# Kernel optimization log

Hardware: AMD Instinct MI355X
Metric: run time of the kernel (lower is better)

Reference implementation:

```python
import jax, jax.numpy as jnp
import numpy as np

STATE_DIM = 256
ACT_LEN = 128
INPUT_DIM = STATE_DIM + 2 * ACT_LEN
B_SZ, T = 32, 2048
SLOPE = 0.01


def leaky(x):
    return jnp.where(x < 0, SLOPE * x, x)


def inv_leaky(x):
    return jnp.where(x < 0, x / SLOPE, x)


def _lin_init(key, out_d, in_d):
    k1, k2 = jax.random.split(key)
    bound = 1.0 / np.sqrt(in_d)
    W = jax.random.uniform(k1, (out_d, in_d), minval=-bound, maxval=bound, dtype=jnp.float32)
    b = jax.random.uniform(k2, (out_d,), minval=-bound, maxval=bound, dtype=jnp.float32)
    return W, b


def setup_inputs() -> dict:
    key = jax.random.key(0)
    ks = jax.random.split(key, 8)
    padded_input = jax.random.normal(ks[0], (B_SZ, T, INPUT_DIM), dtype=jnp.float32)
    We1, be1 = _lin_init(ks[1], STATE_DIM, STATE_DIM)
    We2, be2 = _lin_init(ks[2], STATE_DIM, STATE_DIM)
    A_W, A_b = _lin_init(ks[3], STATE_DIM, STATE_DIM)
    B_W, B_b = _lin_init(ks[4], STATE_DIM, ACT_LEN)
    Wd1, bd1 = _lin_init(ks[5], STATE_DIM, STATE_DIM)
    Wd2, bd2 = _lin_init(ks[6], STATE_DIM, STATE_DIM)
    return {"padded_input": padded_input, "We1": We1, "be1": be1, "We2": We2, "be2": be2,
            "A_W": A_W, "A_b": A_b, "B_W": B_W, "B_b": B_b,
            "Wd1": Wd1, "bd1": bd1, "Wd2": Wd2, "bd2": bd2}


def reference(padded_input, We1, be1, We2, be2, A_W, A_b, B_W, B_b, Wd1, bd1, Wd2, bd2):
    x_t = padded_input[:, :, :STATE_DIM]                      # [B,T,D]
    u_t = padded_input[:, :, STATE_DIM:STATE_DIM + ACT_LEN]   # [B,T,A]
    # encoder: (Linear + LeakyReLU) x 2
    z = leaky(jnp.einsum('btd,ed->bte', x_t, We1) + be1)
    z = leaky(jnp.einsum('btd,ed->bte', z, We2) + be2)
    # recurrence z_{t} uses encoded state only at t=0 (reset_probability=0, nwarmup=0)
    Bu = jnp.einsum('bta,da->btd', u_t, B_W) + B_b            # [B,T,D], precomputed
    z0 = z[:, 0, :]                                           # [B,D]

    def step(carry, bu_t):
        out = jnp.einsum('bd,ed->be', carry, A_W) + A_b + bu_t
        return out, out

    _, z1 = jax.lax.scan(step, z0, jnp.swapaxes(Bu, 0, 1))    # z1: [T,B,D]
    z1 = jnp.swapaxes(z1, 0, 1)                               # [B,T,D]
    # decoder: (InverseLeakyReLU + Linear) x 2
    y = jnp.einsum('btd,ed->bte', inv_leaky(z1), Wd1) + bd1
    y = jnp.einsum('btd,ed->bte', inv_leaky(y), Wd2) + bd2
    return y
```

## Files before the change

kernel.cpp:

```cpp
#include <hip/hip_runtime.h>

#define D256 256
#define ALEN 128
#define INDIM 512
#define BSZ 32
#define TLEN 2048
#define CHL 32
#define NCH 64

typedef __attribute__((ext_vector_type(8))) short short8;
typedef __attribute__((ext_vector_type(4))) float f32x4;

__device__ __forceinline__ float leakyf(float x)  { return x < 0.f ? 0.01f * x : x; }
__device__ __forceinline__ float ileakyf(float x) { return x < 0.f ? x * 100.0f : x; }

__device__ __forceinline__ unsigned short f2bf(float f) {
  unsigned int x = __float_as_uint(f);
  unsigned int r = x + 0x7FFFu + ((x >> 16) & 1u);
  return (unsigned short)(r >> 16);
}

__device__ __forceinline__ float bf2f(unsigned short u) {
  return __uint_as_float(((unsigned int)u) << 16);
}

__device__ __forceinline__ void gload16(const void* g, const void* l) {
  __builtin_amdgcn_global_load_lds(
      (const __attribute__((address_space(1))) unsigned int*)g,
      (__attribute__((address_space(3))) unsigned int*)l, 16, 0, 0);
}

template <int CTRL>
__device__ __forceinline__ float dpp_addf(float x) {
  return x + __int_as_float(__builtin_amdgcn_update_dpp(
                 0, __float_as_int(x), CTRL, 0xF, 0xF, true));
}
__device__ __forceinline__ void red8(float4& s) {
  s.x = dpp_addf<0xB1>(s.x); s.y = dpp_addf<0xB1>(s.y);
  s.z = dpp_addf<0xB1>(s.z); s.w = dpp_addf<0xB1>(s.w);
  s.x = dpp_addf<0x4E>(s.x); s.y = dpp_addf<0x4E>(s.y);
  s.z = dpp_addf<0x4E>(s.z); s.w = dpp_addf<0x4E>(s.w);
  s.x = dpp_addf<0x141>(s.x); s.y = dpp_addf<0x141>(s.y);
  s.z = dpp_addf<0x141>(s.z); s.w = dpp_addf<0x141>(s.w);
}

__global__ __launch_bounds__(256) void gemm_mfma(
    const unsigned short* __restrict__ In, int K,
    const unsigned short* __restrict__ W,
    const float* __restrict__ bias1, const float* __restrict__ bias2,
    int ileaky_act, int out_bf16, void* __restrict__ Outp) {
  __shared__ char lds[16384];
  const int tid = threadIdx.x;
  const int lane = tid & 63, w = tid >> 6;
  const int m0 = blockIdx.x * 128, n0 = blockIdx.y * 128;
  const int wm = (w & 1) * 64, wn = (w >> 1) * 64;
  const int quad = lane >> 4, l16 = lane & 15;

  f32x4 acc[4][4];
#pragma unroll
  for (int i = 0; i < 4; ++i)
#pragma unroll
    for (int j = 0; j < 4; ++j) acc[i][j] = {0.f, 0.f, 0.f, 0.f};

  for (int kb = 0; kb < K; kb += 32) {
    __syncthreads();
#pragma unroll
    for (int q = 0; q < 2; ++q) {
      const int id = (w * 2 + q) * 64 + lane;
      const int row = id >> 2, ch = id & 3;
      gload16(In + (size_t)(m0 + row) * K + kb + ch * 8,
              lds + (w * 2 + q) * 1024);
      gload16(W + (size_t)(n0 + row) * K + kb + ch * 8,
              lds + 8192 + (w * 2 + q) * 1024);
    }
    __syncthreads();

    short8 af[4], bf[4];
#pragma unroll
    for (int i = 0; i < 4; ++i) {
      af[i] = *(const short8*)(lds + ((wm + i * 16 + l16) * 64 + quad * 16));
      bf[i] = *(const short8*)(lds + 8192 + ((wn + i * 16 + l16) * 64 + quad * 16));
    }
#pragma unroll
    for (int i = 0; i < 4; ++i)
#pragma unroll
      for (int j = 0; j < 4; ++j)
        acc[i][j] = __builtin_amdgcn_mfma_f32_16x16x32_bf16(af[i], bf[j], acc[i][j], 0, 0, 0);
  }

#pragma unroll
  for (int j = 0; j < 4; ++j) {
    const int n = n0 + wn + j * 16 + l16;
    const float bv = (bias1 ? bias1[n] : 0.f) + (bias2 ? bias2[n] : 0.f);
#pragma unroll
    for (int i = 0; i < 4; ++i) {
#pragma unroll
      for (int r = 0; r < 4; ++r) {
        const int m = m0 + wm + i * 16 + quad * 4 + r;
        float v = acc[i][j][r] + bv;
        if (ileaky_act) v = ileakyf(v);
        if (out_bf16)
          ((unsigned short*)Outp)[(size_t)m * 256 + n] = f2bf(v);
        else
          ((float*)Outp)[(size_t)m * 256 + n] = v;
      }
    }
  }
}

__global__ __launch_bounds__(256) void gemm_corr(
    const unsigned short* __restrict__ Eb, const unsigned short* __restrict__ Mb,
    const float* __restrict__ Df, unsigned short* __restrict__ w1) {
  __shared__ char lds[16384];
  const int tid = threadIdx.x;
  const int lane = tid & 63, w = tid >> 6;
  const int m0 = blockIdx.x * 128, n0 = blockIdx.y * 128;
  const int wm = (w & 1) * 64, wn = (w >> 1) * 64;
  const int quad = lane >> 4, l16 = lane & 15;

  f32x4 acc[4][4];
#pragma unroll
  for (int i = 0; i < 4; ++i)
#pragma unroll
    for (int j = 0; j < 4; ++j) acc[i][j] = {0.f, 0.f, 0.f, 0.f};

  for (int kb = 0; kb < 256; kb += 32) {
    __syncthreads();
#pragma unroll
    for (int q = 0; q < 2; ++q) {
      const int id = (w * 2 + q) * 64 + lane;
      const int row = id >> 2, ch = id & 3;
      gload16(Eb + (size_t)(m0 + row) * 256 + kb + ch * 8,
              lds + (w * 2 + q) * 1024);
      gload16(Mb + (size_t)(n0 + row) * 256 + kb + ch * 8,
              lds + 8192 + (w * 2 + q) * 1024);
    }
    __syncthreads();

    short8 af[4], bf[4];
#pragma unroll
    for (int i = 0; i < 4; ++i) {
      af[i] = *(const short8*)(lds + ((wm + i * 16 + l16) * 64 + quad * 16));
      bf[i] = *(const short8*)(lds + 8192 + ((wn + i * 16 + l16) * 64 + quad * 16));
    }
#pragma unroll
    for (int i = 0; i < 4; ++i)
#pragma unroll
      for (int j = 0; j < 4; ++j)
        acc[i][j] = __builtin_amdgcn_mfma_f32_16x16x32_bf16(af[i], bf[j], acc[i][j], 0, 0, 0);
  }

#pragma unroll
  for (int jf = 0; jf < 4; ++jf) {
    const int n = n0 + wn + jf * 16 + l16;
    const int jj = n >> 8, e = n & 255;
#pragma unroll
    for (int i = 0; i < 4; ++i) {
#pragma unroll
      for (int r = 0; r < 4; ++r) {
        const int m = m0 + wm + i * 16 + quad * 4 + r;
        const int kk = m >> 5, bb = m & 31;
        const size_t addr = ((size_t)bb * TLEN + (size_t)kk * CHL + jj) * 256 + e;
        float v = acc[i][jf][r] + Df[addr];
        w1[addr] = f2bf(ileakyf(v));
      }
    }
  }
}

__global__ __launch_bounds__(256) void gemm_pow(
    const float* __restrict__ P, const float* __restrict__ XTb,
    float* __restrict__ OutS, float* __restrict__ OutST,
    unsigned short* __restrict__ OutSb) {
  __shared__ float a_lds[64][40];
  __shared__ float b_lds[64][40];
  const size_t zo = (size_t)blockIdx.z << 16;
  const float* XT = XTb + zo;
  const int tid = threadIdx.x;
  const int tm = tid >> 4, tn = tid & 15;
  const int m0 = blockIdx.x * 64, n0 = blockIdx.y * 64;
  float acc[4][4];
#pragma unroll
  for (int i = 0; i < 4; ++i)
#pragma unroll
    for (int j = 0; j < 4; ++j) acc[i][j] = 0.f;

  for (int kb = 0; kb < 256; kb += 32) {
    __syncthreads();
#pragma unroll
    for (int q = 0; q < 2; ++q) {
      const int slot = q * 256 + tid;
      const int row = slot >> 3, s4 = slot & 7;
      *(float4*)&a_lds[row][s4 * 4] = *(const float4*)&P[(size_t)(m0 + row) * 256 + kb + s4 * 4];
      *(float4*)&b_lds[row][s4 * 4] = *(const float4*)&XT[(size_t)(n0 + row) * 256 + kb + s4 * 4];
    }
    __syncthreads();
#pragma unroll
    for (int k4 = 0; k4 < 8; ++k4) {
      float4 a4[4], b4[4];
#pragma unroll
      for (int i = 0; i < 4; ++i) a4[i] = *(const float4*)&a_lds[tm * 4 + i][k4 * 4];
#pragma unroll
      for (int j = 0; j < 4; ++j) b4[j] = *(const float4*)&b_lds[tn * 4 + j][k4 * 4];
#pragma unroll
      for (int i = 0; i < 4; ++i)
#pragma unroll
        for (int j = 0; j < 4; ++j)
          acc[i][j] += a4[i].x * b4[j].x + a4[i].y * b4[j].y +
                       a4[i].z * b4[j].z + a4[i].w * b4[j].w;
    }
  }
  float* Out = OutS + zo;
  float* OutT = OutST + zo;
  unsigned short* Ob = OutSb + zo;
#pragma unroll
  for (int i = 0; i < 4; ++i) {
    const int m = m0 + tm * 4 + i;
    float4 v = make_float4(acc[i][0], acc[i][1], acc[i][2], acc[i][3]);
    *(float4*)&Out[(size_t)m * 256 + n0 + tn * 4] = v;
    *(ushort4*)&Ob[(size_t)m * 256 + n0 + tn * 4] =
        make_ushort4(f2bf(v.x), f2bf(v.y), f2bf(v.z), f2bf(v.w));
#pragma unroll
    for (int j = 0; j < 4; ++j)
      OutT[(size_t)(n0 + tn * 4 + j) * 256 + m] = acc[i][j];
  }
}

__global__ __launch_bounds__(256) void prep_kernel(
    const float* __restrict__ in, const float* __restrict__ We1,
    const float* __restrict__ be1, const float* __restrict__ We2,
    const float* __restrict__ be2, const float* __restrict__ A_W,
    const float* __restrict__ B_W, const float* __restrict__ Wd1,
    const float* __restrict__ Wd2, float* __restrict__ AT0,
    unsigned short* __restrict__ Ab0, float* __restrict__ z0,
    unsigned short* __restrict__ BWb, unsigned short* __restrict__ Wd1b,
    unsigned short* __restrict__ Wd2b) {
  __shared__ float sm[1056];
  const int tid = threadIdx.x;
  const int blk = blockIdx.x;
  if (blk < 64) {
    const int bx = (blk & 7) * 32, by = (blk >> 3) * 32;
    const int lx = tid & 31, ly = tid >> 5;
#pragma unroll
    for (int i = 0; i < 4; ++i) {
      const float v = A_W[(size_t)(by + ly + 8 * i) * 256 + bx + lx];
      sm[(ly + 8 * i) * 33 + lx] = v;
      Ab0[(size_t)(by + ly + 8 * i) * 256 + bx + lx] = f2bf(v);
    }
    __syncthreads();
#pragma unroll
    for (int i = 0; i < 4; ++i)
      AT0[(size_t)(bx + ly + 8 * i) * 256 + by + lx] = sm[lx * 33 + ly + 8 * i];
  } else if (blk < 96) {
    const int b = blk - 64, e = tid;
    float* xb = sm;
    float* h1 = sm + 256;
    xb[e] = in[(size_t)b * TLEN * INDIM + e];
    __syncthreads();
    float acc = be1[e];
    const float4* w = (const float4*)(We1 + (size_t)e * 256);
#pragma unroll 8
    for (int d4 = 0; d4 < 64; ++d4) {
      float4 wv = w[d4];
      acc += wv.x * xb[4 * d4] + wv.y * xb[4 * d4 + 1] + wv.z * xb[4 * d4 + 2] + wv.w * xb[4 * d4 + 3];
    }
    h1[e] = leakyf(acc);
    __syncthreads();
    float a2 = be2[e];
    w = (const float4*)(We2 + (size_t)e * 256);
#pragma unroll 8
    for (int d4 = 0; d4 < 64; ++d4) {
      float4 wv = w[d4];
      a2 += wv.x * h1[4 * d4] + wv.y * h1[4 * d4 + 1] + wv.z * h1[4 * d4 + 2] + wv.w * h1[4 * d4 + 3];
    }
    z0[(size_t)b * 256 + e] = leakyf(a2);
  } else {
    const float* src;
    unsigned short* dst;
    int i4;
    if (blk < 128)      { src = B_W; dst = BWb;  i4 = (blk - 96) * 256 + tid; }
    else if (blk < 192) { src = Wd1; dst = Wd1b; i4 = (blk - 128) * 256 + tid; }
    else                { src = Wd2; dst = Wd2b; i4 = (blk - 192) * 256 + tid; }
    float4 v = *(const float4*)&src[(size_t)i4 * 4];
    *(ushort4*)&dst[(size_t)i4 * 4] =
        make_ushort4(f2bf(v.x), f2bf(v.y), f2bf(v.z), f2bf(v.w));
  }
}

__global__ __launch_bounds__(256) void extract_u(const float* __restrict__ in,
                                                 unsigned short* __restrict__ ubuf) {
  const int gid = blockIdx.x * 256 + threadIdx.x;
  const int row = gid >> 5;
  const int c = (gid & 31) * 4;
  float4 v = *(const float4*)&in[(size_t)row * INDIM + 256 + c];
  *(ushort4*)&ubuf[(size_t)row * 128 + c] =
      make_ushort4(f2bf(v.x), f2bf(v.y), f2bf(v.z), f2bf(v.w));
}

__global__ __launch_bounds__(512, 2) void phase_kernel(
    const float* __restrict__ AW, float* __restrict__ Cbuf,
    float* __restrict__ Lend) {
  const int tid = threadIdx.x;
  const int w = tid >> 6;
  const int lane = tid & 63;
  const int dg = lane & 7;
  const int le = lane >> 3;
  const int e0 = w * 32 + le * 4;
  const int d0 = dg * 32;
  const int rho0 = blockIdx.x << 3;
  const int k = rho0 >> 5;
  const int b = (rho0 & 31) + dg;
  const int rho = rho0 + dg;

  __shared__ __align__(16) float carry[2][8][292];

  float4 Ar[4][8];
#pragma unroll
  for (int i = 0; i < 4; ++i)
#pragma unroll
    for (int k4 = 0; k4 < 8; ++k4)
      Ar[i][k4] = *(const float4*)&AW[(size_t)(e0 + i) * 256 + d0 + k4 * 4];

  float4 cur = make_float4(0.f, 0.f, 0.f, 0.f);
  const int epad = e0 + ((e0 >> 5) << 2);
  *(float4*)&carry[0][dg][epad] = cur;
  __syncthreads();

  float4* crow = (float4*)(Cbuf + ((size_t)b * TLEN + (size_t)k * CHL) * 256 + e0);

  int buf = 0;
  for (int j = 0; j < CHL; ++j) {
    const float4 cj = *crow;
    float4 s[8];
#pragma unroll
    for (int r = 0; r < 8; ++r) s[r] = make_float4(0.f, 0.f, 0.f, 0.f);
#pragma unroll
    for (int k4 = 0; k4 < 8; ++k4) {
      const float4 a0 = Ar[0][k4], a1 = Ar[1][k4], a2 = Ar[2][k4], a3 = Ar[3][k4];
#pragma unroll
      for (int r = 0; r < 8; ++r) {
        const float4 cv = *(const float4*)&carry[buf][r][dg * 36 + k4 * 4];
        s[r].x += a0.x * cv.x + a0.y * cv.y + a0.z * cv.z + a0.w * cv.w;
        s[r].y += a1.x * cv.x + a1.y * cv.y + a1.z * cv.z + a1.w * cv.w;
        s[r].z += a2.x * cv.x + a2.y * cv.y + a2.z * cv.z + a2.w * cv.w;
        s[r].w += a3.x * cv.x + a3.y * cv.y + a3.z * cv.z + a3.w * cv.w;
      }
    }
    float4 nxt = make_float4(0.f, 0.f, 0.f, 0.f);
#pragma unroll
    for (int r = 0; r < 8; ++r) {
      red8(s[r]);
      if (dg == r) nxt = s[r];
    }
    cur = make_float4(nxt.x + cj.x, nxt.y + cj.y, nxt.z + cj.z, nxt.w + cj.w);
    buf ^= 1;
    *(float4*)&carry[buf][dg][epad] = cur;
    *crow = cur;
    crow += 64;
    __syncthreads();
  }
  *(float4*)&Lend[(size_t)rho * 256 + e0] = cur;
}

__global__ __launch_bounds__(512, 2) void boundary_kernel(
    const float* __restrict__ P, const float* __restrict__ z0,
    const float* __restrict__ Lend, unsigned short* __restrict__ Eb) {
  const int tid = threadIdx.x;
  const int w = tid >> 6;
  const int lane = tid & 63;
  const int dg = lane & 7;
  const int le = lane >> 3;
  const int e0 = w * 32 + le * 4;
  const int d0 = dg * 32;
  const int b = blockIdx.x;

  __shared__ __align__(16) float Ec[292];

  float4 Pr[4][8];
#pragma unroll
  for (int i = 0; i < 4; ++i)
#pragma unroll
    for (int k4 = 0; k4 < 8; ++k4)
      Pr[i][k4] = *(const float4*)&P[(size_t)(e0 + i) * 256 + d0 + k4 * 4];

  float4 cur = *(const float4*)&z0[(size_t)b * 256 + e0];
  const int epad = e0 + ((e0 >> 5) << 2);
  if (dg == 0) *(float4*)&Ec[epad] = cur;
  __syncthreads();

  for (int k = 0; k < NCH; ++k) {
    const float4 lv = *(const float4*)&Lend[((size_t)k * BSZ + b) * 256 + e0];
    if (dg == 0)
      *(ushort4*)&Eb[((size_t)k * BSZ + b) * 256 + e0] =
          make_ushort4(f2bf(cur.x), f2bf(cur.y), f2bf(cur.z), f2bf(cur.w));

    float4 s = make_float4(0.f, 0.f, 0.f, 0.f);
#pragma unroll
    for (int k4 = 0; k4 < 8; ++k4) {
      const float4 cv = *(const float4*)&Ec[dg * 36 + k4 * 4];
      s.x += Pr[0][k4].x * cv.x + Pr[0][k4].y * cv.y + Pr[0][k4].z * cv.z + Pr[0][k4].w * cv.w;
      s.y += Pr[1][k4].x * cv.x + Pr[1][k4].y * cv.y + Pr[1][k4].z * cv.z + Pr[1][k4].w * cv.w;
      s.z += Pr[2][k4].x * cv.x + Pr[2][k4].y * cv.y + Pr[2][k4].z * cv.z + Pr[2][k4].w * cv.w;
      s.w += Pr[3][k4].x * cv.x + Pr[3][k4].y * cv.y + Pr[3][k4].z * cv.z + Pr[3][k4].w * cv.w;
    }
    red8(s);
    cur = make_float4(s.x + lv.x, s.y + lv.y, s.z + lv.z, s.w + lv.w);
    __syncthreads();
    if (dg == 0) *(float4*)&Ec[epad] = cur;
    __syncthreads();
  }
}

extern "C" void kernel_launch(void* const* d_in, const int* in_sizes, int n_in,
                              void* d_out, int out_size, void* d_ws, size_t ws_size,
                              hipStream_t stream) {
  const float* in  = (const float*)d_in[0];
  const float* We1 = (const float*)d_in[1];
  const float* be1 = (const float*)d_in[2];
  const float* We2 = (const float*)d_in[3];
  const float* be2 = (const float*)d_in[4];
  const float* A_W = (const float*)d_in[5];
  const float* A_b = (const float*)d_in[6];
  const float* B_W = (const float*)d_in[7];
  const float* B_b = (const float*)d_in[8];
  const float* Wd1 = (const float*)d_in[9];
  const float* bd1 = (const float*)d_in[10];
  const float* Wd2 = (const float*)d_in[11];
  const float* bd2 = (const float*)d_in[12];
  float* out = (float*)d_out;

  float* ws     = (float*)d_ws;
  float* Cbuf   = ws;
  float* Mstack = Cbuf + 16777216;
  float* z0     = Mstack + 2097152;
  float* Lend   = z0 + 8192;
  unsigned short* Mstackb = (unsigned short*)(Lend + 524288);
  unsigned short* Eb   = Mstackb + 2097152;
  unsigned short* BWb  = Eb + 524288;
  unsigned short* Wd1b = BWb + 32768;
  unsigned short* Wd2b = Wd1b + 65536;
  float* MstackT = Cbuf;

  unsigned short* ubuf = (unsigned short*)d_out;
  unsigned short* w1   = ubuf + 8388608;
  unsigned short* w2   = (unsigned short*)Cbuf;

  prep_kernel<<<256, 256, 0, stream>>>(in, We1, be1, We2, be2, A_W, B_W, Wd1,
                                       Wd2, MstackT, Mstackb, z0, BWb, Wd1b, Wd2b);

  gemm_pow<<<dim3(4, 4, 1),  256, 0, stream>>>(A_W,                 MstackT, Mstack + 1 * 65536,  MstackT + 1 * 65536,  Mstackb + 1 * 65536);
  gemm_pow<<<dim3(4, 4, 2),  256, 0, stream>>>(Mstack + 1 * 65536,  MstackT, Mstack + 2 * 65536,  MstackT + 2 * 65536,  Mstackb + 2 * 65536);
  gemm_pow<<<dim3(4, 4, 4),  256, 0, stream>>>(Mstack + 3 * 65536,  MstackT, Mstack + 4 * 65536,  MstackT + 4 * 65536,  Mstackb + 4 * 65536);
  gemm_pow<<<dim3(4, 4, 8),  256, 0, stream>>>(Mstack + 7 * 65536,  MstackT, Mstack + 8 * 65536,  MstackT + 8 * 65536,  Mstackb + 8 * 65536);
  gemm_pow<<<dim3(4, 4, 16), 256, 0, stream>>>(Mstack + 15 * 65536, MstackT, Mstack + 16 * 65536, MstackT + 16 * 65536, Mstackb + 16 * 65536);

  extract_u<<<8192, 256, 0, stream>>>(in, ubuf);

  gemm_mfma<<<dim3(512, 2), 256, 0, stream>>>(ubuf, ALEN, BWb, A_b, B_b, 0, 0, Cbuf);

  phase_kernel<<<256, 512, 0, stream>>>(A_W, Cbuf, Lend);
  boundary_kernel<<<32, 512, 0, stream>>>(Mstack + 31 * 65536, z0, Lend, Eb);
  gemm_corr<<<dim3(16, 64), 256, 0, stream>>>(Eb, Mstackb, Cbuf, w1);

  gemm_mfma<<<dim3(512, 2), 256, 0, stream>>>(w1, D256, Wd1b, bd1, nullptr, 1, 1, w2);
  gemm_mfma<<<dim3(512, 2), 256, 0, stream>>>(w2, D256, Wd2b, bd2, nullptr, 0, 0, out);
}
```

Baseline: 757.6 us.

## Stage GEMM epilogues through LDS and keep recurrence partials in bf16

GEMM epilogues now write the accumulator tiles into a padded LDS buffer and re-read them row-wise. Each thread then emits 16 contiguous outputs with vector stores, replacing the scattered per-element stores with wide coalesced ones. The phase kernel now writes its chunk-local recurrence results as bf16 into the w1 buffer instead of overwriting the fp32 Cbuf. gemm_corr updates w1 in place, which roughly halves the bytes it reads and writes for the correction term. The trade-offs are an extra bf16 rounding of the intermediate state before the correction is added, plus extra LDS use and barriers in the epilogues.

```diff
diff --git a/kernel.cpp b/kernel.cpp
--- a/kernel.cpp
+++ b/kernel.cpp
@@ -10,6 +10,7 @@
 
 typedef __attribute__((ext_vector_type(8))) short short8;
 typedef __attribute__((ext_vector_type(4))) float f32x4;
+typedef __attribute__((ext_vector_type(8))) unsigned short u16x8;
 
 __device__ __forceinline__ float leakyf(float x)  { return x < 0.f ? 0.01f * x : x; }
 __device__ __forceinline__ float ileakyf(float x) { return x < 0.f ? x * 100.0f : x; }
@@ -50,6 +51,7 @@
     const float* __restrict__ bias1, const float* __restrict__ bias2,
     int ileaky_act, int out_bf16, void* __restrict__ Outp) {
   __shared__ char lds[16384];
+  __shared__ float ldsF[32][132];
   const int tid = threadIdx.x;
   const int lane = tid & 63, w = tid >> 6;
   const int m0 = blockIdx.x * 128, n0 = blockIdx.y * 128;
@@ -88,30 +90,65 @@
         acc[i][j] = __builtin_amdgcn_mfma_f32_16x16x32_bf16(af[i], bf[j], acc[i][j], 0, 0, 0);
   }
 
-#pragma unroll
-  for (int j = 0; j < 4; ++j) {
-    const int n = n0 + wn + j * 16 + l16;
-    const float bv = (bias1 ? bias1[n] : 0.f) + (bias2 ? bias2[n] : 0.f);
-#pragma unroll
-    for (int i = 0; i < 4; ++i) {
-#pragma unroll
-      for (int r = 0; r < 4; ++r) {
-        const int m = m0 + wm + i * 16 + quad * 4 + r;
-        float v = acc[i][j][r] + bv;
-        if (ileaky_act) v = ileakyf(v);
-        if (out_bf16)
-          ((unsigned short*)Outp)[(size_t)m * 256 + n] = f2bf(v);
-        else
-          ((float*)Outp)[(size_t)m * 256 + n] = v;
+  const int lrow = tid >> 3, c0 = (tid & 7) * 16;
+#pragma unroll
+  for (int p = 0; p < 4; ++p) {
+    if ((w & 1) == (p >> 1)) {
+      const int ib = 2 * (p & 1);
+#pragma unroll
+      for (int ii = 0; ii < 2; ++ii)
+#pragma unroll
+        for (int j = 0; j < 4; ++j)
+#pragma unroll
+          for (int r = 0; r < 4; ++r)
+            ldsF[ii * 16 + quad * 4 + r][wn + j * 16 + l16] = acc[ib + ii][j][r];
+    }
+    __syncthreads();
+    const int m = m0 + p * 32 + lrow;
+    const int nb = n0 + c0;
+    float v[16];
+#pragma unroll
+    for (int k = 0; k < 4; ++k) {
+      const float4 b1 = *(const float4*)&bias1[nb + 4 * k];
+#pragma unroll
+      for (int c = 0; c < 4; ++c) v[4 * k + c] = ldsF[lrow][c0 + 4 * k + c] + ((const float*)&b1)[c];
+    }
+    if (bias2) {
+#pragma unroll
+      for (int k = 0; k < 4; ++k) {
+        const float4 b2 = *(const float4*)&bias2[nb + 4 * k];
+#pragma unroll
+        for (int c = 0; c < 4; ++c) v[4 * k + c] += ((const float*)&b2)[c];
       }
     }
+    if (ileaky_act) {
+#pragma unroll
+      for (int c = 0; c < 16; ++c) v[c] = ileakyf(v[c]);
+    }
+    if (out_bf16) {
+      unsigned short* op = (unsigned short*)Outp + (size_t)m * 256 + nb;
+#pragma unroll
+      for (int h = 0; h < 2; ++h) {
+        u16x8 ov;
+#pragma unroll
+        for (int c = 0; c < 8; ++c) ov[c] = f2bf(v[h * 8 + c]);
+        *(u16x8*)(op + h * 8) = ov;
+      }
+    } else {
+      float* op = (float*)Outp + (size_t)m * 256 + nb;
+#pragma unroll
+      for (int k = 0; k < 4; ++k)
+        *(float4*)(op + 4 * k) = make_float4(v[4 * k], v[4 * k + 1], v[4 * k + 2], v[4 * k + 3]);
+    }
+    __syncthreads();
   }
 }
 
 __global__ __launch_bounds__(256) void gemm_corr(
     const unsigned short* __restrict__ Eb, const unsigned short* __restrict__ Mb,
-    const float* __restrict__ Df, unsigned short* __restrict__ w1) {
+    unsigned short* w1 ) {
   __shared__ char lds[16384];
+  __shared__ float ldsF[32][132];
   const int tid = threadIdx.x;
   const int lane = tid & 63, w = tid >> 6;
   const int m0 = blockIdx.x * 128, n0 = blockIdx.y * 128;
@@ -150,21 +187,37 @@
         acc[i][j] = __builtin_amdgcn_mfma_f32_16x16x32_bf16(af[i], bf[j], acc[i][j], 0, 0, 0);
   }
 
-#pragma unroll
-  for (int jf = 0; jf < 4; ++jf) {
-    const int n = n0 + wn + jf * 16 + l16;
-    const int jj = n >> 8, e = n & 255;
-#pragma unroll
-    for (int i = 0; i < 4; ++i) {
-#pragma unroll
-      for (int r = 0; r < 4; ++r) {
-        const int m = m0 + wm + i * 16 + quad * 4 + r;
-        const int kk = m >> 5, bb = m & 31;
-        const size_t addr = ((size_t)bb * TLEN + (size_t)kk * CHL + jj) * 256 + e;
-        float v = acc[i][jf][r] + Df[addr];
-        w1[addr] = f2bf(ileakyf(v));
+  const int lrow = tid >> 3, c0 = (tid & 7) * 16;
+#pragma unroll
+  for (int p = 0; p < 4; ++p) {
+    if ((w & 1) == (p >> 1)) {
+      const int ib = 2 * (p & 1);
+#pragma unroll
+      for (int ii = 0; ii < 2; ++ii)
+#pragma unroll
+        for (int j = 0; j < 4; ++j)
+#pragma unroll
+          for (int r = 0; r < 4; ++r)
+            ldsF[ii * 16 + quad * 4 + r][wn + j * 16 + l16] = acc[ib + ii][j][r];
+    }
+    __syncthreads();
+    const int m = m0 + p * 32 + lrow;
+    const int kk = m >> 5, bb = m & 31;
+    const int nb = n0 + c0;
+    const int jj = nb >> 8, e = nb & 255;
+    const size_t addr = ((size_t)bb * TLEN + (size_t)kk * CHL + jj) * 256 + e;
+#pragma unroll
+    for (int h = 0; h < 2; ++h) {
+      const u16x8 dv = *(const u16x8*)&w1[addr + h * 8];
+      u16x8 ov;
+#pragma unroll
+      for (int c = 0; c < 8; ++c) {
+        float v = ldsF[lrow][c0 + h * 8 + c] + bf2f(dv[c]);
+        ov[c] = f2bf(ileakyf(v));
       }
-    }
+      *(u16x8*)&w1[addr + h * 8] = ov;
+    }
+    __syncthreads();
   }
 }
 
@@ -298,8 +351,8 @@
 }
 
 __global__ __launch_bounds__(512, 2) void phase_kernel(
-    const float* __restrict__ AW, float* __restrict__ Cbuf,
-    float* __restrict__ Lend) {
+    const float* __restrict__ AW, const float* __restrict__ Cbuf,
+    float* __restrict__ Lend, unsigned short* __restrict__ dout) {
   const int tid = threadIdx.x;
   const int w = tid >> 6;
   const int lane = tid & 63;
@@ -326,11 +379,13 @@
   *(float4*)&carry[0][dg][epad] = cur;
   __syncthreads();
 
-  float4* crow = (float4*)(Cbuf + ((size_t)b * TLEN + (size_t)k * CHL) * 256 + e0);
+  const float4* crow = (const float4*)(Cbuf + ((size_t)b * TLEN + (size_t)k * CHL) * 256 + e0);
+  ushort4* wrow = (ushort4*)(dout + ((size_t)b * TLEN + (size_t)k * CHL) * 256 + e0);
 
   int buf = 0;
   for (int j = 0; j < CHL; ++j) {
     const float4 cj = *crow;
+    crow += 64;
     float4 s[8];
 #pragma unroll
     for (int r = 0; r < 8; ++r) s[r] = make_float4(0.f, 0.f, 0.f, 0.f);
@@ -355,8 +410,8 @@
     cur = make_float4(nxt.x + cj.x, nxt.y + cj.y, nxt.z + cj.z, nxt.w + cj.w);
     buf ^= 1;
     *(float4*)&carry[buf][dg][epad] = cur;
-    *crow = cur;
-    crow += 64;
+    *wrow = make_ushort4(f2bf(cur.x), f2bf(cur.y), f2bf(cur.z), f2bf(cur.w));
+    wrow += 64;
     __syncthreads();
   }
   *(float4*)&Lend[(size_t)rho * 256 + e0] = cur;
@@ -458,9 +513,9 @@
 
   gemm_mfma<<<dim3(512, 2), 256, 0, stream>>>(ubuf, ALEN, BWb, A_b, B_b, 0, 0, Cbuf);
 
-  phase_kernel<<<256, 512, 0, stream>>>(A_W, Cbuf, Lend);
+  phase_kernel<<<256, 512, 0, stream>>>(A_W, Cbuf, Lend, w1);
   boundary_kernel<<<32, 512, 0, stream>>>(Mstack + 31 * 65536, z0, Lend, Eb);
-  gemm_corr<<<dim3(16, 64), 256, 0, stream>>>(Eb, Mstackb, Cbuf, w1);
+  gemm_corr<<<dim3(16, 64), 256, 0, stream>>>(Eb, Mstackb, w1);
 
   gemm_mfma<<<dim3(512, 2), 256, 0, stream>>>(w1, D256, Wd1b, bd1, nullptr, 1, 1, w2);
   gemm_mfma<<<dim3(512, 2), 256, 0, stream>>>(w2, D256, Wd2b, bd2, nullptr, 0, 0, out);
```

Result: slower. 847.0 us (+11.8%).
